# Optimization experiments

Measured on AMD Instinct MI355X. Metric: run time of the kernel, lower is better.

Reference implementation:

```python
import jax, jax.numpy as jnp
import numpy as np

N = 100000
E = 1600000
DIN = 64
DH = 64
C = 16


def _sage_conv(x, edge_index, W_l, W_r, b):
    # PyG SAGEConv (aggr='mean'): out = lin_l(mean_{j in N(i)} x_j) + lin_r(x_i)
    src, dst = edge_index[0], edge_index[1]
    msgs = x[src]                                   # [E, D] gather
    num_nodes = x.shape[0]
    agg = jax.ops.segment_sum(msgs, dst, num_segments=num_nodes)      # [N, D]
    deg = jax.ops.segment_sum(jnp.ones((msgs.shape[0],), x.dtype), dst,
                              num_segments=num_nodes)                 # [N]
    mean = agg / jnp.maximum(deg, 1.0)[:, None]
    return mean @ W_l + b + x @ W_r


def setup_inputs() -> dict:
    key = jax.random.key(0)
    ks = jax.random.split(key, 8)
    x = jax.random.normal(ks[0], (N, DIN), dtype=jnp.float32)
    edge_index = jax.random.randint(ks[1], (2, E), 0, N, dtype=jnp.int64)
    s = 1.0 / np.sqrt(DIN)
    W1_l = jax.random.normal(ks[2], (DIN, DH), dtype=jnp.float32) * s
    W1_r = jax.random.normal(ks[3], (DIN, DH), dtype=jnp.float32) * s
    b1 = jnp.zeros((DH,), jnp.float32)
    sh = 1.0 / np.sqrt(DH)
    W2_l = jax.random.normal(ks[4], (DH, C), dtype=jnp.float32) * sh
    W2_r = jax.random.normal(ks[5], (DH, C), dtype=jnp.float32) * sh
    b2 = jnp.zeros((C,), jnp.float32)
    return {"x": x, "edge_index": edge_index, "W1_l": W1_l, "W1_r": W1_r,
            "b1": b1, "W2_l": W2_l, "W2_r": W2_r, "b2": b2}


def reference(x, edge_index, W1_l, W1_r, b1, W2_l, W2_r, b2):
    h = _sage_conv(x, edge_index, W1_l, W1_r, b1)
    h = jax.nn.relu(h)
    # dropout is identity at inference
    out = _sage_conv(h, edge_index, W2_l, W2_r, b2)
    return out
```

## Files before the change

kernel.cpp:

```cpp
#include <hip/hip_runtime.h>

#define NB 256
#define CHUNK 8192

__global__ void k_init(int* __restrict__ gcur, int capE) {
  gcur[threadIdx.x] = threadIdx.x * capE;
}

__global__ void k_part(const int* __restrict__ srcI, const int* __restrict__ dstI,
                       int* __restrict__ gcur, int2* __restrict__ pairs,
                       int E, int N, int capN, int capE) {
  __shared__ int hist[NB];
  __shared__ int base[NB];
  __shared__ int cnt[NB];
  int tid = threadIdx.x;
  int e0 = blockIdx.x * CHUNK;
  int eend = min(e0 + CHUNK, E);
  hist[tid] = 0;
  __syncthreads();
  for (int e = e0 + tid; e < eend; e += 256) {
    int d = dstI[e];
    if ((unsigned)d < (unsigned)N) atomicAdd(&hist[d / capN], 1);
  }
  __syncthreads();
  base[tid] = atomicAdd(&gcur[tid], hist[tid]);
  cnt[tid] = 0;
  __syncthreads();
  for (int e = e0 + tid; e < eend; e += 256) {
    int d = dstI[e];
    int s = srcI[e];
    if ((unsigned)d < (unsigned)N && (unsigned)s < (unsigned)N) {
      int b = d / capN;
      int slot = base[b] + atomicAdd(&cnt[b], 1);
      if (slot < (b + 1) * capE)
        pairs[slot] = make_int2(d, s);
    }
  }
}

__launch_bounds__(512)
__global__ void k_csr(const int2* __restrict__ pairs, const int* __restrict__ gcur,
                      int* __restrict__ deg, int* __restrict__ rowoff,
                      int* __restrict__ csr, int N, int capN, int capE) {
  __shared__ int hist[512];
  __shared__ int tmp[512];
  __shared__ int cur[512];
  int q = blockIdx.x;
  int tid = threadIdx.x;
  int nloc = N - q * capN;
  if (nloc > capN) nloc = capN;
  int base = q * capE;
  int cnt = gcur[q] - base;
  if (cnt > capE) cnt = capE;
  int qbase = q * capN;
  hist[tid] = 0;
  __syncthreads();
  for (int e = tid; e < cnt; e += 512) {
    int2 pr = pairs[base + e];
    int dl = pr.x - qbase;
    if ((unsigned)dl < (unsigned)nloc && (unsigned)pr.y < (unsigned)N)
      atomicAdd(&hist[dl], 1);
  }
  __syncthreads();
  int v = hist[tid];
  tmp[tid] = v;
  __syncthreads();
  for (int off = 1; off < 512; off <<= 1) {
    int t = (tid >= off) ? tmp[tid - off] : 0;
    __syncthreads();
    tmp[tid] += t;
    __syncthreads();
  }
  int ex = tmp[tid] - v;
  cur[tid] = ex;
  if (tid < nloc) {
    int i = qbase + tid;
    deg[i] = v;
    rowoff[i] = base + ex;
  }
  __syncthreads();
  for (int e = tid; e < cnt; e += 512) {
    int2 pr = pairs[base + e];
    int dl = pr.x - qbase;
    if ((unsigned)dl < (unsigned)nloc && (unsigned)pr.y < (unsigned)N) {
      int pos = atomicAdd(&cur[dl], 1);
      csr[base + pos] = pr.y;
    }
  }
}

__global__ void k_agg64(const float* __restrict__ x, const int* __restrict__ csr,
                        const int* __restrict__ rowoff, const int* __restrict__ deg,
                        float* __restrict__ m, int n) {
  int w = (blockIdx.x * blockDim.x + threadIdx.x) >> 6;
  int lane = threadIdx.x & 63;
  if (w >= n) return;
  int start = __builtin_amdgcn_readfirstlane(rowoff[w]);
  int d = __builtin_amdgcn_readfirstlane(deg[w]);
  float a0 = 0.f, a1 = 0.f, a2 = 0.f, a3 = 0.f;
  int j = 0;
  for (; j + 3 < d; j += 4) {
    int s0 = csr[start + j];
    int s1 = csr[start + j + 1];
    int s2 = csr[start + j + 2];
    int s3 = csr[start + j + 3];
    a0 += x[(size_t)s0 * 64 + lane];
    a1 += x[(size_t)s1 * 64 + lane];
    a2 += x[(size_t)s2 * 64 + lane];
    a3 += x[(size_t)s3 * 64 + lane];
  }
  for (; j < d; ++j) a0 += x[(size_t)csr[start + j] * 64 + lane];
  float inv = (d > 0) ? 1.f / (float)d : 0.f;
  m[(size_t)w * 64 + lane] = ((a0 + a1) + (a2 + a3)) * inv;
}

__launch_bounds__(256, 4)
__global__ void k_h(const float* __restrict__ m, const float* __restrict__ x,
                    const float* __restrict__ Wl, const float* __restrict__ Wr,
                    const float* __restrict__ b1, float* __restrict__ h, int n) {
  __shared__ float sAT[32 * 68];
  __shared__ float sW[32 * 64];
  int tid = threadIdx.x;
  int row0 = blockIdx.x * 64;
  int colT = tid & 15;
  int rowT = tid >> 4;
  float acc[4][4];
#pragma unroll
  for (int r = 0; r < 4; ++r)
#pragma unroll
    for (int c = 0; c < 4; ++c) acc[r][c] = 0.f;

  for (int kt = 0; kt < 4; ++kt) {
    const float* asrc = (kt < 2) ? m : x;
    const float* wsrc = (kt < 2) ? Wl : Wr;
    int ko = (kt & 1) * 32;
    __syncthreads();
    {
      int f = tid;
#pragma unroll
      for (int i = 0; i < 2; ++i, f += 256) {
        int r = f >> 3, kq = f & 7;
        int rr = row0 + r; if (rr > n - 1) rr = n - 1;
        float4 v = *(const float4*)(asrc + (size_t)rr * 64 + ko + kq * 4);
        sAT[(kq * 4 + 0) * 68 + r] = v.x;
        sAT[(kq * 4 + 1) * 68 + r] = v.y;
        sAT[(kq * 4 + 2) * 68 + r] = v.z;
        sAT[(kq * 4 + 3) * 68 + r] = v.w;
      }
      int g = tid;
#pragma unroll
      for (int i = 0; i < 2; ++i, g += 256) {
        int wr = g >> 4, cq = g & 15;
        float4 v = *(const float4*)(wsrc + (size_t)(ko + wr) * 64 + cq * 4);
        *(float4*)&sW[wr * 64 + cq * 4] = v;
      }
    }
    __syncthreads();
#pragma unroll 4
    for (int k = 0; k < 32; ++k) {
      float4 a = *(const float4*)&sAT[k * 68 + rowT * 4];
      float4 w = *(const float4*)&sW[k * 64 + colT * 4];
      acc[0][0] += a.x * w.x; acc[0][1] += a.x * w.y; acc[0][2] += a.x * w.z; acc[0][3] += a.x * w.w;
      acc[1][0] += a.y * w.x; acc[1][1] += a.y * w.y; acc[1][2] += a.y * w.z; acc[1][3] += a.y * w.w;
      acc[2][0] += a.z * w.x; acc[2][1] += a.z * w.y; acc[2][2] += a.z * w.z; acc[2][3] += a.z * w.w;
      acc[3][0] += a.w * w.x; acc[3][1] += a.w * w.y; acc[3][2] += a.w * w.z; acc[3][3] += a.w * w.w;
    }
  }
  float4 bb = *(const float4*)(b1 + colT * 4);
#pragma unroll
  for (int r = 0; r < 4; ++r) {
    int row = row0 + rowT * 4 + r;
    if (row < n) {
      float4 o;
      o.x = fmaxf(acc[r][0] + bb.x, 0.f);
      o.y = fmaxf(acc[r][1] + bb.y, 0.f);
      o.z = fmaxf(acc[r][2] + bb.z, 0.f);
      o.w = fmaxf(acc[r][3] + bb.w, 0.f);
      *(float4*)(h + (size_t)row * 64 + colT * 4) = o;
    }
  }
}

__launch_bounds__(256, 4)
__global__ void k_pq(const float* __restrict__ h, const float* __restrict__ W2l,
                     const float* __restrict__ W2r, float* __restrict__ p,
                     float* __restrict__ q, int n) {
  __shared__ float sAT[32 * 132];
  __shared__ float sW[32 * 32];
  int tid = threadIdx.x;
  int row0 = blockIdx.x * 128;
  int colT = tid & 7;
  int rowT = tid >> 3;
  float acc[4][4];
#pragma unroll
  for (int r = 0; r < 4; ++r)
#pragma unroll
    for (int c = 0; c < 4; ++c) acc[r][c] = 0.f;

  for (int kt = 0; kt < 2; ++kt) {
    int ko = kt * 32;
    __syncthreads();
    {
      int f = tid;
#pragma unroll
      for (int i = 0; i < 4; ++i, f += 256) {
        int r = f >> 3, kq = f & 7;
        int rr = row0 + r; if (rr > n - 1) rr = n - 1;
        float4 v = *(const float4*)(h + (size_t)rr * 64 + ko + kq * 4);
        sAT[(kq * 4 + 0) * 132 + r] = v.x;
        sAT[(kq * 4 + 1) * 132 + r] = v.y;
        sAT[(kq * 4 + 2) * 132 + r] = v.z;
        sAT[(kq * 4 + 3) * 132 + r] = v.w;
      }
      int wr = tid >> 3, cq = tid & 7;
      const float* wsrc = (cq < 4) ? W2l : W2r;
      int cc = (cq & 3) * 4;
      float4 v = *(const float4*)(wsrc + (size_t)(ko + wr) * 16 + cc);
      *(float4*)&sW[wr * 32 + cq * 4] = v;
    }
    __syncthreads();
#pragma unroll 4
    for (int k = 0; k < 32; ++k) {
      float4 a = *(const float4*)&sAT[k * 132 + rowT * 4];
      float4 w = *(const float4*)&sW[k * 32 + colT * 4];
      acc[0][0] += a.x * w.x; acc[0][1] += a.x * w.y; acc[0][2] += a.x * w.z; acc[0][3] += a.x * w.w;
      acc[1][0] += a.y * w.x; acc[1][1] += a.y * w.y; acc[1][2] += a.y * w.z; acc[1][3] += a.y * w.w;
      acc[2][0] += a.z * w.x; acc[2][1] += a.z * w.y; acc[2][2] += a.z * w.z; acc[2][3] += a.z * w.w;
      acc[3][0] += a.w * w.x; acc[3][1] += a.w * w.y; acc[3][2] += a.w * w.z; acc[3][3] += a.w * w.w;
    }
  }
#pragma unroll
  for (int r = 0; r < 4; ++r) {
    int row = row0 + rowT * 4 + r;
    if (row < n) {
      float* dst = (colT < 4) ? (p + (size_t)row * 16 + colT * 4)
                              : (q + (size_t)row * 16 + (colT - 4) * 4);
      *(float4*)dst = make_float4(acc[r][0], acc[r][1], acc[r][2], acc[r][3]);
    }
  }
}

__global__ void k_agg16(const float* __restrict__ p, const int* __restrict__ csr,
                        const int* __restrict__ rowoff, const int* __restrict__ deg,
                        const float* __restrict__ b2, float* __restrict__ out, int n) {
  int t = blockIdx.x * blockDim.x + threadIdx.x;
  int i = t >> 4;
  int dd = t & 15;
  if (i >= n) return;
  int start = rowoff[i];
  int d = deg[i];
  float a0 = 0.f, a1 = 0.f, a2 = 0.f, a3 = 0.f;
  int j = 0;
  for (; j + 3 < d; j += 4) {
    int s0 = csr[start + j];
    int s1 = csr[start + j + 1];
    int s2 = csr[start + j + 2];
    int s3 = csr[start + j + 3];
    a0 += p[(size_t)s0 * 16 + dd];
    a1 += p[(size_t)s1 * 16 + dd];
    a2 += p[(size_t)s2 * 16 + dd];
    a3 += p[(size_t)s3 * 16 + dd];
  }
  for (; j < d; ++j) a0 += p[(size_t)csr[start + j] * 16 + dd];
  float inv = (d > 0) ? 1.f / (float)d : 0.f;
  out[t] = ((a0 + a1) + (a2 + a3)) * inv + out[t] + b2[dd];
}

extern "C" void kernel_launch(void* const* d_in, const int* in_sizes, int n_in,
                              void* d_out, int out_size, void* d_ws, size_t ws_size,
                              hipStream_t stream) {
  const float* x   = (const float*)d_in[0];
  const int*   ei  = (const int*)d_in[1];
  const float* W1l = (const float*)d_in[2];
  const float* W1r = (const float*)d_in[3];
  const float* b1  = (const float*)d_in[4];
  const float* W2l = (const float*)d_in[5];
  const float* W2r = (const float*)d_in[6];
  const float* b2  = (const float*)d_in[7];
  float* out = (float*)d_out;

  int N = in_sizes[0] / 64;
  int E = in_sizes[1] / 2;
  const int* srcI = ei;
  const int* dstI = ei + E;

  int capN = (N + NB - 1) / NB;
  int capE = E / NB + 1024;

  size_t off = 0;
  auto alloc = [&](size_t bytes) -> char* {
    char* r = (char*)d_ws + off;
    off = (off + bytes + 255) & ~(size_t)255;
    return r;
  };
  int*   deg    = (int*)alloc((size_t)N * 4);
  int*   rowoff = (int*)alloc((size_t)N * 4);
  int*   csr    = (int*)alloc((size_t)NB * capE * 4);
  int*   gcur   = (int*)alloc(NB * 4);
  float* m      = (float*)alloc((size_t)N * 64 * 4);
  float* h      = (float*)alloc((size_t)N * 64 * 4);
  float* p      = (float*)alloc((size_t)N * 16 * 4);
  int2*  pairs  = (int2*)m;
  if (off > ws_size) return;
  if ((size_t)NB * capE * 8 > (size_t)N * 64 * 4) return;

  k_init<<<1, NB, 0, stream>>>(gcur, capE);
  k_part<<<(E + CHUNK - 1) / CHUNK, 256, 0, stream>>>(srcI, dstI, gcur, pairs, E, N, capN, capE);
  k_csr<<<NB, 512, 0, stream>>>(pairs, gcur, deg, rowoff, csr, N, capN, capE);

  k_agg64<<<(N * 64 + 255) / 256, 256, 0, stream>>>(x, csr, rowoff, deg, m, N);
  k_h<<<(N + 63) / 64, 256, 0, stream>>>(m, x, W1l, W1r, b1, h, N);

  k_pq<<<(N + 127) / 128, 256, 0, stream>>>(h, W2l, W2r, p, out, N);
  k_agg16<<<(N * 16 + 255) / 256, 256, 0, stream>>>(p, csr, rowoff, deg, b2, out, N);
}
```

Baseline: 256.9 us.

## Fuse layer-1 mean aggregation into GEMM kernel and pack edge pairs

Merges the 64-wide neighbour-mean gather into the first-layer GEMM kernel, so the aggregated rows stay in shared memory and the intermediate m buffer is never written or re-read. Edge (dst,src) pairs are packed into one 32-bit word, which halves partition traffic. k_init is replaced by a memset. The gather loops are unrolled to 8 for more memory-level parallelism. Risks: each block now gathers 64 rows with only 4 waves, and that serial loop may lower the parallelism available to hide latency. The packing also requires N ≤ 2^17 and capN ≤ 512.

```diff
diff --git a/kernel.cpp b/kernel.cpp
--- a/kernel.cpp
+++ b/kernel.cpp
@@ -3,12 +3,8 @@
 #define NB 256
 #define CHUNK 8192
 
-__global__ void k_init(int* __restrict__ gcur, int capE) {
-  gcur[threadIdx.x] = threadIdx.x * capE;
-}
-
 __global__ void k_part(const int* __restrict__ srcI, const int* __restrict__ dstI,
-                       int* __restrict__ gcur, int2* __restrict__ pairs,
+                       int* __restrict__ gcur, int* __restrict__ pairs,
                        int E, int N, int capN, int capE) {
   __shared__ int hist[NB];
   __shared__ int base[NB];
@@ -23,7 +19,7 @@
     if ((unsigned)d < (unsigned)N) atomicAdd(&hist[d / capN], 1);
   }
   __syncthreads();
-  base[tid] = atomicAdd(&gcur[tid], hist[tid]);
+  base[tid] = tid * capE + atomicAdd(&gcur[tid], hist[tid]);
   cnt[tid] = 0;
   __syncthreads();
   for (int e = e0 + tid; e < eend; e += 256) {
@@ -33,13 +29,13 @@
       int b = d / capN;
       int slot = base[b] + atomicAdd(&cnt[b], 1);
       if (slot < (b + 1) * capE)
-        pairs[slot] = make_int2(d, s);
+        pairs[slot] = ((d - b * capN) << 17) | s;
     }
   }
 }
 
 __launch_bounds__(512)
-__global__ void k_csr(const int2* __restrict__ pairs, const int* __restrict__ gcur,
+__global__ void k_csr(const int* __restrict__ pairs, const int* __restrict__ gcur,
                       int* __restrict__ deg, int* __restrict__ rowoff,
                       int* __restrict__ csr, int N, int capN, int capE) {
   __shared__ int hist[512];
@@ -50,16 +46,15 @@
   int nloc = N - q * capN;
   if (nloc > capN) nloc = capN;
   int base = q * capE;
-  int cnt = gcur[q] - base;
+  int cnt = gcur[q];
   if (cnt > capE) cnt = capE;
   int qbase = q * capN;
   hist[tid] = 0;
   __syncthreads();
   for (int e = tid; e < cnt; e += 512) {
-    int2 pr = pairs[base + e];
-    int dl = pr.x - qbase;
-    if ((unsigned)dl < (unsigned)nloc && (unsigned)pr.y < (unsigned)N)
-      atomicAdd(&hist[dl], 1);
+    int code = pairs[base + e];
+    int dl = (unsigned)code >> 17;
+    if (dl < nloc) atomicAdd(&hist[dl], 1);
   }
   __syncthreads();
   int v = hist[tid];
@@ -80,48 +75,58 @@
   }
   __syncthreads();
   for (int e = tid; e < cnt; e += 512) {
-    int2 pr = pairs[base + e];
-    int dl = pr.x - qbase;
-    if ((unsigned)dl < (unsigned)nloc && (unsigned)pr.y < (unsigned)N) {
+    int code = pairs[base + e];
+    int dl = (unsigned)code >> 17;
+    if (dl < nloc) {
       int pos = atomicAdd(&cur[dl], 1);
-      csr[base + pos] = pr.y;
-    }
-  }
-}
-
-__global__ void k_agg64(const float* __restrict__ x, const int* __restrict__ csr,
-                        const int* __restrict__ rowoff, const int* __restrict__ deg,
-                        float* __restrict__ m, int n) {
-  int w = (blockIdx.x * blockDim.x + threadIdx.x) >> 6;
-  int lane = threadIdx.x & 63;
-  if (w >= n) return;
-  int start = __builtin_amdgcn_readfirstlane(rowoff[w]);
-  int d = __builtin_amdgcn_readfirstlane(deg[w]);
-  float a0 = 0.f, a1 = 0.f, a2 = 0.f, a3 = 0.f;
-  int j = 0;
-  for (; j + 3 < d; j += 4) {
-    int s0 = csr[start + j];
-    int s1 = csr[start + j + 1];
-    int s2 = csr[start + j + 2];
-    int s3 = csr[start + j + 3];
-    a0 += x[(size_t)s0 * 64 + lane];
-    a1 += x[(size_t)s1 * 64 + lane];
-    a2 += x[(size_t)s2 * 64 + lane];
-    a3 += x[(size_t)s3 * 64 + lane];
-  }
-  for (; j < d; ++j) a0 += x[(size_t)csr[start + j] * 64 + lane];
-  float inv = (d > 0) ? 1.f / (float)d : 0.f;
-  m[(size_t)w * 64 + lane] = ((a0 + a1) + (a2 + a3)) * inv;
+      csr[base + pos] = code & 0x1FFFF;
+    }
+  }
 }
 
 __launch_bounds__(256, 4)
-__global__ void k_h(const float* __restrict__ m, const float* __restrict__ x,
-                    const float* __restrict__ Wl, const float* __restrict__ Wr,
-                    const float* __restrict__ b1, float* __restrict__ h, int n) {
-  __shared__ float sAT[32 * 68];
-  __shared__ float sW[32 * 64];
+__global__ void k_aggh(const float* __restrict__ x, const int* __restrict__ csr,
+                       const int* __restrict__ rowoff, const int* __restrict__ deg,
+                       const float* __restrict__ W1l, const float* __restrict__ W1r,
+                       const float* __restrict__ b1, float* __restrict__ h, int n) {
+  __shared__ float sM[64 * 68];
+  __shared__ float sX[32 * 68];
   int tid = threadIdx.x;
   int row0 = blockIdx.x * 64;
+  int wid = tid >> 6;
+  int lane = tid & 63;
+
+  for (int r16 = 0; r16 < 16; ++r16) {
+    int row = row0 + wid * 16 + r16;
+    if (row >= n) break;
+    int start = __builtin_amdgcn_readfirstlane(rowoff[row]);
+    int d = __builtin_amdgcn_readfirstlane(deg[row]);
+    float a0 = 0.f, a1 = 0.f, a2 = 0.f, a3 = 0.f;
+    float a4 = 0.f, a5 = 0.f, a6 = 0.f, a7 = 0.f;
+    int j = 0;
+    for (; j + 7 < d; j += 8) {
+      int s0 = csr[start + j], s1 = csr[start + j + 1];
+      int s2 = csr[start + j + 2], s3 = csr[start + j + 3];
+      int s4 = csr[start + j + 4], s5 = csr[start + j + 5];
+      int s6 = csr[start + j + 6], s7 = csr[start + j + 7];
+      a0 += x[(size_t)s0 * 64 + lane]; a1 += x[(size_t)s1 * 64 + lane];
+      a2 += x[(size_t)s2 * 64 + lane]; a3 += x[(size_t)s3 * 64 + lane];
+      a4 += x[(size_t)s4 * 64 + lane]; a5 += x[(size_t)s5 * 64 + lane];
+      a6 += x[(size_t)s6 * 64 + lane]; a7 += x[(size_t)s7 * 64 + lane];
+    }
+    for (; j + 3 < d; j += 4) {
+      int s0 = csr[start + j], s1 = csr[start + j + 1];
+      int s2 = csr[start + j + 2], s3 = csr[start + j + 3];
+      a0 += x[(size_t)s0 * 64 + lane]; a1 += x[(size_t)s1 * 64 + lane];
+      a2 += x[(size_t)s2 * 64 + lane]; a3 += x[(size_t)s3 * 64 + lane];
+    }
+    for (; j < d; ++j) a0 += x[(size_t)csr[start + j] * 64 + lane];
+    float inv = (d > 0) ? 1.f / (float)d : 0.f;
+    sM[lane * 68 + wid * 16 + r16] =
+        (((a0 + a1) + (a2 + a3)) + ((a4 + a5) + (a6 + a7))) * inv;
+  }
+  __syncthreads();
+
   int colT = tid & 15;
   int rowT = tid >> 4;
   float acc[4][4];
@@ -131,35 +136,31 @@
     for (int c = 0; c < 4; ++c) acc[r][c] = 0.f;
 
   for (int kt = 0; kt < 4; ++kt) {
-    const float* asrc = (kt < 2) ? m : x;
-    const float* wsrc = (kt < 2) ? Wl : Wr;
+    const float* wsrc = (kt < 2) ? W1l : W1r;
     int ko = (kt & 1) * 32;
-    __syncthreads();
-    {
+    const float* abase;
+    if (kt < 2) {
+      abase = &sM[ko * 68];
+    } else {
+      __syncthreads();
       int f = tid;
 #pragma unroll
       for (int i = 0; i < 2; ++i, f += 256) {
         int r = f >> 3, kq = f & 7;
         int rr = row0 + r; if (rr > n - 1) rr = n - 1;
-        float4 v = *(const float4*)(asrc + (size_t)rr * 64 + ko + kq * 4);
-        sAT[(kq * 4 + 0) * 68 + r] = v.x;
-        sAT[(kq * 4 + 1) * 68 + r] = v.y;
-        sAT[(kq * 4 + 2) * 68 + r] = v.z;
-        sAT[(kq * 4 + 3) * 68 + r] = v.w;
+        float4 v = *(const float4*)(x + (size_t)rr * 64 + ko + kq * 4);
+        sX[(kq * 4 + 0) * 68 + r] = v.x;
+        sX[(kq * 4 + 1) * 68 + r] = v.y;
+        sX[(kq * 4 + 2) * 68 + r] = v.z;
+        sX[(kq * 4 + 3) * 68 + r] = v.w;
       }
-      int g = tid;
-#pragma unroll
-      for (int i = 0; i < 2; ++i, g += 256) {
-        int wr = g >> 4, cq = g & 15;
-        float4 v = *(const float4*)(wsrc + (size_t)(ko + wr) * 64 + cq * 4);
-        *(float4*)&sW[wr * 64 + cq * 4] = v;
-      }
-    }
-    __syncthreads();
+      __syncthreads();
+      abase = sX;
+    }
 #pragma unroll 4
     for (int k = 0; k < 32; ++k) {
-      float4 a = *(const float4*)&sAT[k * 68 + rowT * 4];
-      float4 w = *(const float4*)&sW[k * 64 + colT * 4];
+      float4 a = *(const float4*)&abase[k * 68 + rowT * 4];
+      float4 w = *(const float4*)(wsrc + (size_t)(ko + k) * 64 + colT * 4);
       acc[0][0] += a.x * w.x; acc[0][1] += a.x * w.y; acc[0][2] += a.x * w.z; acc[0][3] += a.x * w.w;
       acc[1][0] += a.y * w.x; acc[1][1] += a.y * w.y; acc[1][2] += a.y * w.z; acc[1][3] += a.y * w.w;
       acc[2][0] += a.z * w.x; acc[2][1] += a.z * w.y; acc[2][2] += a.z * w.z; acc[2][3] += a.z * w.w;
@@ -250,20 +251,27 @@
   int start = rowoff[i];
   int d = deg[i];
   float a0 = 0.f, a1 = 0.f, a2 = 0.f, a3 = 0.f;
+  float a4 = 0.f, a5 = 0.f, a6 = 0.f, a7 = 0.f;
   int j = 0;
+  for (; j + 7 < d; j += 8) {
+    int s0 = csr[start + j], s1 = csr[start + j + 1];
+    int s2 = csr[start + j + 2], s3 = csr[start + j + 3];
+    int s4 = csr[start + j + 4], s5 = csr[start + j + 5];
+    int s6 = csr[start + j + 6], s7 = csr[start + j + 7];
+    a0 += p[(size_t)s0 * 16 + dd]; a1 += p[(size_t)s1 * 16 + dd];
+    a2 += p[(size_t)s2 * 16 + dd]; a3 += p[(size_t)s3 * 16 + dd];
+    a4 += p[(size_t)s4 * 16 + dd]; a5 += p[(size_t)s5 * 16 + dd];
+    a6 += p[(size_t)s6 * 16 + dd]; a7 += p[(size_t)s7 * 16 + dd];
+  }
   for (; j + 3 < d; j += 4) {
-    int s0 = csr[start + j];
-    int s1 = csr[start + j + 1];
-    int s2 = csr[start + j + 2];
-    int s3 = csr[start + j + 3];
-    a0 += p[(size_t)s0 * 16 + dd];
-    a1 += p[(size_t)s1 * 16 + dd];
-    a2 += p[(size_t)s2 * 16 + dd];
-    a3 += p[(size_t)s3 * 16 + dd];
+    int s0 = csr[start + j], s1 = csr[start + j + 1];
+    int s2 = csr[start + j + 2], s3 = csr[start + j + 3];
+    a0 += p[(size_t)s0 * 16 + dd]; a1 += p[(size_t)s1 * 16 + dd];
+    a2 += p[(size_t)s2 * 16 + dd]; a3 += p[(size_t)s3 * 16 + dd];
   }
   for (; j < d; ++j) a0 += p[(size_t)csr[start + j] * 16 + dd];
   float inv = (d > 0) ? 1.f / (float)d : 0.f;
-  out[t] = ((a0 + a1) + (a2 + a3)) * inv + out[t] + b2[dd];
+  out[t] = ((((a0 + a1) + (a2 + a3)) + ((a4 + a5) + (a6 + a7)))) * inv + out[t] + b2[dd];
 }
 
 extern "C" void kernel_launch(void* const* d_in, const int* in_sizes, int n_in,
@@ -297,19 +305,18 @@
   int*   rowoff = (int*)alloc((size_t)N * 4);
   int*   csr    = (int*)alloc((size_t)NB * capE * 4);
   int*   gcur   = (int*)alloc(NB * 4);
-  float* m      = (float*)alloc((size_t)N * 64 * 4);
   float* h      = (float*)alloc((size_t)N * 64 * 4);
   float* p      = (float*)alloc((size_t)N * 16 * 4);
-  int2*  pairs  = (int2*)m;
+  int*   pairs  = (int*)h;
   if (off > ws_size) return;
-  if ((size_t)NB * capE * 8 > (size_t)N * 64 * 4) return;
-
-  k_init<<<1, NB, 0, stream>>>(gcur, capE);
+  if ((size_t)NB * capE * 4 > (size_t)N * 64 * 4) return;
+  if (N > (1 << 17) || capN > (1 << 9)) return;
+
+  hipMemsetAsync(gcur, 0, NB * 4, stream);
   k_part<<<(E + CHUNK - 1) / CHUNK, 256, 0, stream>>>(srcI, dstI, gcur, pairs, E, N, capN, capE);
   k_csr<<<NB, 512, 0, stream>>>(pairs, gcur, deg, rowoff, csr, N, capN, capE);
 
-  k_agg64<<<(N * 64 + 255) / 256, 256, 0, stream>>>(x, csr, rowoff, deg, m, N);
-  k_h<<<(N + 63) / 64, 256, 0, stream>>>(m, x, W1l, W1r, b1, h, N);
+  k_aggh<<<(N + 63) / 64, 256, 0, stream>>>(x, csr, rowoff, deg, W1l, W1r, b1, h, N);
 
   k_pq<<<(N + 127) / 128, 256, 0, stream>>>(h, W2l, W2r, p, out, N);
   k_agg16<<<(N * 16 + 255) / 256, 256, 0, stream>>>(p, csr, rowoff, deg, b2, out, N);
```

Result: slower. 272.5 us (+6.1%).
